# Kernel tuning notes

Hardware: AMD Instinct MI355X
Metric: run time of the kernel (lower is better)

## Reference

```python
import jax, jax.numpy as jnp
import numpy as np

N_NODES = 100000
N_EDGES = 1600000
IN_DIM, HID, OUT_DIM = 512, 32, 40


def setup_inputs() -> dict:
    key = jax.random.key(0)
    ks = jax.random.split(key, 6)
    x = jax.random.normal(ks[0], (N_NODES, IN_DIM), dtype=jnp.float32)
    edge_index = jax.random.randint(ks[1], (2, N_EDGES), 0, N_NODES, dtype=jnp.int64)
    # Glorot-ish init for the linear weights
    W1 = jax.random.normal(ks[2], (IN_DIM, HID), dtype=jnp.float32) / np.sqrt(IN_DIM)
    b1 = jnp.zeros((HID,), dtype=jnp.float32)
    W2 = jax.random.normal(ks[3], (HID, OUT_DIM), dtype=jnp.float32) / np.sqrt(HID)
    b2 = jnp.zeros((OUT_DIM,), dtype=jnp.float32)
    return {"x": x, "edge_index": edge_index, "W1": W1, "b1": b1, "W2": W2, "b2": b2}


def gcn_conv(x, W, b, src, dst, n_nodes):
    """PyG GCNConv: h = D^{-1/2} (A + I) D^{-1/2} (x W) + b."""
    h = x @ W  # linear transform first (reduces edge-level traffic)
    # add self-loops
    loop = jnp.arange(n_nodes, dtype=src.dtype)
    s = jnp.concatenate([src, loop])
    d = jnp.concatenate([dst, loop])
    # symmetric normalization from in-degree (including self-loops)
    deg = jax.ops.segment_sum(jnp.ones_like(d, dtype=h.dtype), d, num_segments=n_nodes)
    dinv = jnp.where(deg > 0, jax.lax.rsqrt(deg), 0.0)
    norm = dinv[s] * dinv[d]  # [E+N]
    msg = h[s] * norm[:, None]  # gather + scale
    out = jax.ops.segment_sum(msg, d, num_segments=n_nodes)  # scatter-add
    return out + b


def reference(x, edge_index, W1, b1, W2, b2):
    src, dst = edge_index[0], edge_index[1]
    n = x.shape[0]
    h = jax.nn.relu(gcn_conv(x, W1, b1, src, dst, n))
    # dropout is identity in eval mode (reference runs in eval)
    out = gcn_conv(h, W2, b2, src, dst, n)
    return out
```

## Files before the change

### kernel.cpp

```cpp
#include <hip/hip_runtime.h>
#include <hip/hip_bf16.h>

#define N_IN 512
#define HID 32
#define OUTD 40

typedef __attribute__((ext_vector_type(8))) short bf16x8;
typedef __attribute__((ext_vector_type(4))) float f32x4;


__global__ void k_init(int* __restrict__ csr, int tot4, int n4, int n,
                       float* __restrict__ g1, float* __restrict__ p,
                       int* __restrict__ cnt)
{
    int i = blockIdx.x * blockDim.x + threadIdx.x;
    if (i < tot4) {
        int4 v = make_int4(n, n, n, n);
        *(int4*)&csr[(size_t)i * 4] = v;
    }
    if (i < n4) {
        int4 z4 = make_int4(0, 0, 0, 0);
        *(int4*)&cnt[(size_t)i * 4] = z4;
    }
    if (blockIdx.x == 0) {
        float4 z = make_float4(0.f, 0.f, 0.f, 0.f);
        if (threadIdx.x < 8)
            *(float4*)&g1[(size_t)n * HID + threadIdx.x * 4] = z;
        else if (threadIdx.x < 16)
            *(float4*)&p[(size_t)n * HID + (threadIdx.x - 8) * 4] = z;
    }
}

__global__ void k_count(const int* __restrict__ dst, int* cnt, int e) {
    int i = (blockIdx.x * blockDim.x + threadIdx.x) * 4;
    if (i + 3 < e) {
        int4 d4 = *(const int4*)&dst[i];
        atomicAdd(&cnt[d4.x], 1);
        atomicAdd(&cnt[d4.y], 1);
        atomicAdd(&cnt[d4.z], 1);
        atomicAdd(&cnt[d4.w], 1);
    } else {
        for (int k = i; k < e; k++) atomicAdd(&cnt[dst[k]], 1);
    }
}

__global__ __launch_bounds__(256) void k_scan1(const int* __restrict__ cnt,
                                               int* __restrict__ offs,
                                               int* __restrict__ bsums, int n)
{
    __shared__ int sm[256];
    int t = threadIdx.x;
    int base = blockIdx.x * 1024 + t * 4;
    int a0 = (base + 0 < n) ? cnt[base + 0] : 0;
    int a1 = (base + 1 < n) ? cnt[base + 1] : 0;
    int a2 = (base + 2 < n) ? cnt[base + 2] : 0;
    int a3 = (base + 3 < n) ? cnt[base + 3] : 0;
    int d0 = (a0 + 15) & ~15;
    int d1 = (a1 + 15) & ~15;
    int d2 = (a2 + 15) & ~15;
    int d3 = (a3 + 15) & ~15;
    int s = d0 + d1 + d2 + d3;
    sm[t] = s;
    __syncthreads();
#pragma unroll
    for (int off = 1; off < 256; off <<= 1) {
        int v = (t >= off) ? sm[t - off] : 0;
        __syncthreads();
        sm[t] += v;
        __syncthreads();
    }
    int excl = sm[t] - s;
    if (base + 0 < n) offs[base + 0] = excl;
    if (base + 1 < n) offs[base + 1] = excl + d0;
    if (base + 2 < n) offs[base + 2] = excl + d0 + d1;
    if (base + 3 < n) offs[base + 3] = excl + d0 + d1 + d2;
    if (t == 255) bsums[blockIdx.x] = sm[255];
}

__global__ __launch_bounds__(256) void k_scan2(int* bsums, int nb)
{
    __shared__ int sm[256];
    int t = threadIdx.x;
    int s = (t < nb) ? bsums[t] : 0;
    sm[t] = s;
    __syncthreads();
#pragma unroll
    for (int off = 1; off < 256; off <<= 1) {
        int v = (t >= off) ? sm[t - off] : 0;
        __syncthreads();
        sm[t] += v;
        __syncthreads();
    }
    if (t < nb) bsums[t] = sm[t] - s;
}

__global__ void k_scan3(int* __restrict__ offs, int* __restrict__ cursor,
                        const int* __restrict__ bsums, const int* __restrict__ cnt,
                        float* __restrict__ dinv, int n)
{
    int i = blockIdx.x * blockDim.x + threadIdx.x;
    if (i >= n) return;
    int o = offs[i] + bsums[i >> 10];
    offs[i] = o;
    cursor[i] = o;
    dinv[i] = rsqrtf((float)(cnt[i] + 1));
}

__global__ void k_fill(const int* __restrict__ src, const int* __restrict__ dst,
                       int* cursor, int* __restrict__ csr, int e)
{
    int i = (blockIdx.x * blockDim.x + threadIdx.x) * 4;
    if (i >= e) return;
    if (i + 3 < e) {
        int4 d4 = *(const int4*)&dst[i];
        int4 s4 = *(const int4*)&src[i];
        int dd[4] = {d4.x, d4.y, d4.z, d4.w};
        int ss[4] = {s4.x, s4.y, s4.z, s4.w};
#pragma unroll
        for (int k = 0; k < 4; k++) {
            int p = atomicAdd(&cursor[dd[k]], 1);
            csr[p] = ss[k];
        }
    } else {
        for (int k = i; k < e; k++) {
            int p = atomicAdd(&cursor[dst[k]], 1);
            csr[p] = src[k];
        }
    }
}

__global__ void k_convw(const float* __restrict__ W, unsigned short* __restrict__ wfh,
                        unsigned short* __restrict__ wfl)
{
    int idx = blockIdx.x * blockDim.x + threadIdx.x;
    int j     = idx & 7;
    int lane  = (idx >> 3) & 63;
    int ntile = (idx >> 9) & 1;
    int kstep = idx >> 10;
    int k    = kstep * 32 + (lane >> 4) * 8 + j;
    int ncol = ntile * 16 + (lane & 15);
    float v = W[k * HID + ncol];
    unsigned u = __builtin_bit_cast(unsigned, v);
    unsigned short h = (unsigned short)(u >> 16);
    float hv = __builtin_bit_cast(float, u & 0xFFFF0000u);
    float rem = v - hv;
    unsigned ur = __builtin_bit_cast(unsigned, rem);
    ur += 0x7FFF + ((ur >> 16) & 1);
    wfh[idx] = h;
    wfl[idx] = (unsigned short)(ur >> 16);
}

__global__ __launch_bounds__(256) void k_gemm1(
    const float* __restrict__ x,
    const unsigned short* __restrict__ wfh, const unsigned short* __restrict__ wfl,
    const float* __restrict__ dinv, float* __restrict__ g1, int n)
{
    const int t    = threadIdx.x;
    const int lane = t & 63;
    const int wave = t >> 6;
    const int m    = lane & 15;
    const int quad = lane >> 4;
    const int row0 = blockIdx.x * 64 + wave * 16;

    int arow = row0 + m;
    if (arow >= n) arow = n - 1;
    const float* xp = x + (size_t)arow * N_IN + quad * 8;

    f32x4 acc0 = {0.f, 0.f, 0.f, 0.f};
    f32x4 acc1 = {0.f, 0.f, 0.f, 0.f};

    for (int ks = 0; ks < 16; ks++) {
        float4 xa = *(const float4*)(xp + ks * 32);
        float4 xb = *(const float4*)(xp + ks * 32 + 4);
        float xe[8] = {xa.x, xa.y, xa.z, xa.w, xb.x, xb.y, xb.z, xb.w};
        bf16x8 ah, al;
#pragma unroll
        for (int j = 0; j < 8; j++) {
            unsigned u = __builtin_bit_cast(unsigned, xe[j]);
            ah[j] = (short)(u >> 16);
            float hv = __builtin_bit_cast(float, u & 0xFFFF0000u);
            float rem = xe[j] - hv;
            unsigned ur = __builtin_bit_cast(unsigned, rem);
            ur += 0x7FFF + ((ur >> 16) & 1);
            al[j] = (short)(ur >> 16);
        }
        bf16x8 bh0 = *(const bf16x8*)(wfh + ((size_t)(ks * 2 + 0) * 64 + lane) * 8);
        bf16x8 bh1 = *(const bf16x8*)(wfh + ((size_t)(ks * 2 + 1) * 64 + lane) * 8);
        bf16x8 bl0 = *(const bf16x8*)(wfl + ((size_t)(ks * 2 + 0) * 64 + lane) * 8);
        bf16x8 bl1 = *(const bf16x8*)(wfl + ((size_t)(ks * 2 + 1) * 64 + lane) * 8);

        acc0 = __builtin_amdgcn_mfma_f32_16x16x32_bf16(ah, bh0, acc0, 0, 0, 0);
        acc0 = __builtin_amdgcn_mfma_f32_16x16x32_bf16(al, bh0, acc0, 0, 0, 0);
        acc0 = __builtin_amdgcn_mfma_f32_16x16x32_bf16(ah, bl0, acc0, 0, 0, 0);
        acc1 = __builtin_amdgcn_mfma_f32_16x16x32_bf16(ah, bh1, acc1, 0, 0, 0);
        acc1 = __builtin_amdgcn_mfma_f32_16x16x32_bf16(al, bh1, acc1, 0, 0, 0);
        acc1 = __builtin_amdgcn_mfma_f32_16x16x32_bf16(ah, bl1, acc1, 0, 0, 0);
    }

#pragma unroll
    for (int r = 0; r < 4; r++) {
        int row = row0 + quad * 4 + r;
        if (row < n) {
            float dv = dinv[row];
            g1[(size_t)row * HID + m]      = acc0[r] * dv;
            g1[(size_t)row * HID + 16 + m] = acc1[r] * dv;
        }
    }
}


__global__ void k_agg1(const int* __restrict__ csr, const int* __restrict__ offs,
                       const int* __restrict__ cnt, const float* __restrict__ g,
                       const float* __restrict__ dinv, const float* __restrict__ b1,
                       float* __restrict__ p, int n)
{
    int gid = blockIdx.x * blockDim.x + threadIdx.x;
    int r  = gid >> 4;
    int sl = gid & 15;
    if (r >= n) return;
    int s0 = offs[r];
    int dp = (cnt[r] + 15) & ~15;
    int half = sl >> 3;
    int c = sl & 7;
    const float* gc = g + c * 4;
    float4 acc = make_float4(0.f, 0.f, 0.f, 0.f);
    if (half == 0) acc = *(const float4*)&gc[(size_t)r * HID];
    for (int b = 0; b < dp; b += 16) {
        int s = csr[s0 + b + sl];
#pragma unroll
        for (int jj = 0; jj < 8; jj++) {
            int sj = __shfl(s, jj + (half << 3), 16);
            float4 v = *(const float4*)&gc[(size_t)sj * HID];
            acc.x += v.x; acc.y += v.y; acc.z += v.z; acc.w += v.w;
        }
    }
    float4 o;
    o.x = __shfl(acc.x, sl ^ 8, 16);
    o.y = __shfl(acc.y, sl ^ 8, 16);
    o.z = __shfl(acc.z, sl ^ 8, 16);
    o.w = __shfl(acc.w, sl ^ 8, 16);
    if (half == 0) {
        float dv = dinv[r];
        float4 bv = *(const float4*)&b1[c * 4];
        float4 hp;
        hp.x = dv * fmaxf((acc.x + o.x) * dv + bv.x, 0.f);
        hp.y = dv * fmaxf((acc.y + o.y) * dv + bv.y, 0.f);
        hp.z = dv * fmaxf((acc.z + o.z) * dv + bv.z, 0.f);
        hp.w = dv * fmaxf((acc.w + o.w) * dv + bv.w, 0.f);
        *(float4*)&p[(size_t)r * HID + c * 4] = hp;
    }
}

__global__ void k_agg2_out(const int* __restrict__ csr, const int* __restrict__ offs,
                           const int* __restrict__ cnt, const float* __restrict__ g,
                           const float* __restrict__ dinv, const float* __restrict__ W2,
                           const float* __restrict__ b2, float* __restrict__ out, int n)
{
    int gid = blockIdx.x * blockDim.x + threadIdx.x;
    int r  = gid >> 4;
    int sl = gid & 15;
    if (r >= n) return;
    int s0 = offs[r];
    int dp = (cnt[r] + 15) & ~15;
    int half = sl >> 3;
    int c = sl & 7;
    const float* gc = g + c * 4;
    float4 acc = make_float4(0.f, 0.f, 0.f, 0.f);
    if (half == 0) acc = *(const float4*)&gc[(size_t)r * HID];
    for (int b = 0; b < dp; b += 16) {
        int s = csr[s0 + b + sl];
#pragma unroll
        for (int jj = 0; jj < 8; jj++) {
            int sj = __shfl(s, jj + (half << 3), 16);
            float4 v = *(const float4*)&gc[(size_t)sj * HID];
            acc.x += v.x; acc.y += v.y; acc.z += v.z; acc.w += v.w;
        }
    }
    float4 o;
    o.x = __shfl(acc.x, sl ^ 8, 16);
    o.y = __shfl(acc.y, sl ^ 8, 16);
    o.z = __shfl(acc.z, sl ^ 8, 16);
    o.w = __shfl(acc.w, sl ^ 8, 16);
    float dv = dinv[r];
    float h0 = (acc.x + o.x) * dv;
    float h1 = (acc.y + o.y) * dv;
    float h2 = (acc.z + o.z) * dv;
    float h3 = (acc.w + o.w) * dv;

    int oc = (sl < 10) ? sl * 4 : 0;
    float4 ov = *(const float4*)&b2[oc];
#pragma unroll
    for (int k4 = 0; k4 < 8; k4++) {
        float a0 = __shfl(h0, k4, 16);
        float a1 = __shfl(h1, k4, 16);
        float a2 = __shfl(h2, k4, 16);
        float a3 = __shfl(h3, k4, 16);
        float4 w0 = *(const float4*)&W2[(4 * k4 + 0) * OUTD + oc];
        float4 w1 = *(const float4*)&W2[(4 * k4 + 1) * OUTD + oc];
        float4 w2 = *(const float4*)&W2[(4 * k4 + 2) * OUTD + oc];
        float4 w3 = *(const float4*)&W2[(4 * k4 + 3) * OUTD + oc];
        ov.x += a0 * w0.x + a1 * w1.x + a2 * w2.x + a3 * w3.x;
        ov.y += a0 * w0.y + a1 * w1.y + a2 * w2.y + a3 * w3.y;
        ov.z += a0 * w0.z + a1 * w1.z + a2 * w2.z + a3 * w3.z;
        ov.w += a0 * w0.w + a1 * w1.w + a2 * w2.w + a3 * w3.w;
    }
    if (sl < 10) *(float4*)&out[(size_t)r * OUTD + sl * 4] = ov;
}

extern "C" void kernel_launch(void* const* d_in, const int* in_sizes, int n_in,
                              void* d_out, int out_size, void* d_ws, size_t ws_size,
                              hipStream_t stream)
{
    const float* x  = (const float*)d_in[0];
    const int*   ei = (const int*)d_in[1];
    const float* W1 = (const float*)d_in[2];
    const float* b1 = (const float*)d_in[3];
    const float* W2 = (const float*)d_in[4];
    const float* b2 = (const float*)d_in[5];
    float* out = (float*)d_out;

    const int n = in_sizes[0] / N_IN;
    const int e = in_sizes[1] / 2;
    const int* src = ei;
    const int* dst = ei + e;

    const int csr_cap = e + 16 * n;

    char* w = (char*)d_ws;
    float* dinv   = (float*)w;            w += sizeof(float) * (size_t)((n + 3) & ~3);
    float* g1     = (float*)w;            w += sizeof(float) * (size_t)(n + 1) * HID;
    float* p      = (float*)w;            w += sizeof(float) * (size_t)(n + 1) * HID;
    int*   cnt    = (int*)w;              w += sizeof(int) * (size_t)((n + 3) & ~3);
    int*   offs   = (int*)w;              w += sizeof(int) * (size_t)((n + 3) & ~3);
    int*   cursor = (int*)w;              w += sizeof(int) * (size_t)((n + 3) & ~3);
    int*   bsums  = (int*)w;              w += sizeof(int) * 1024;
    unsigned short* wfh = (unsigned short*)w;  w += sizeof(unsigned short) * 16384;
    unsigned short* wfl = (unsigned short*)w;  w += sizeof(unsigned short) * 16384;
    int*   csr    = (int*)w;              w += sizeof(int) * (size_t)((csr_cap + 3) & ~3);

    const int nb = (n + 1023) / 1024;
    const int ec = (e + 3) / 4;
    const int n4 = (n + 3) / 4;
    const int tot4 = (csr_cap + 3) / 4;
    const int initN = (tot4 > n4) ? tot4 : n4;

    k_init<<<(initN + 255) / 256, 256, 0, stream>>>(csr, tot4, n4, n, g1, p, cnt);
    k_count<<<(ec + 255) / 256, 256, 0, stream>>>(dst, cnt, e);
    k_scan1<<<nb, 256, 0, stream>>>(cnt, offs, bsums, n);
    k_scan2<<<1, 256, 0, stream>>>(bsums, nb);
    k_scan3<<<(n + 255) / 256, 256, 0, stream>>>(offs, cursor, bsums, cnt, dinv, n);
    k_fill<<<(ec + 255) / 256, 256, 0, stream>>>(src, dst, cursor, csr, e);

    k_convw<<<64, 256, 0, stream>>>(W1, wfh, wfl);

    k_gemm1<<<(n + 63) / 64, 256, 0, stream>>>(x, wfh, wfl, dinv, g1, n);

    int t16 = n * 16;
    k_agg1<<<(t16 + 255) / 256, 256, 0, stream>>>(csr, offs, cnt, g1, dinv, b1, p, n);
    k_agg2_out<<<(t16 + 255) / 256, 256, 0, stream>>>(csr, offs, cnt, p, dinv, W2, b2, out, n);
}
```

Measured before the change: 596.1 us.

## Privatize degree counters and record atomic ranks to remove fill-phase atomics

Degree counting now uses eight privatized counter copies selected by block index, and each edge records its copy id and returned atomic rank. A per-node pass turns the copies into per-copy bases, and a new position kernel computes each edge's CSR slot from offset, base and rank. The fill then scatters without atomics. This aims to cut atomic contention and drop the second atomic pass over a cursor array, at the cost of extra kernels, an E-sized rank buffer and more memory traffic.

```diff
diff --git a/kernel.cpp b/kernel.cpp
--- a/kernel.cpp
+++ b/kernel.cpp
@@ -4,23 +4,23 @@
 #define N_IN 512
 #define HID 32
 #define OUTD 40
+#define NCOPY 8
 
 typedef __attribute__((ext_vector_type(8))) short bf16x8;
 typedef __attribute__((ext_vector_type(4))) float f32x4;
 
 
-__global__ void k_init(int* __restrict__ csr, int tot4, int n4, int n,
-                       float* __restrict__ g1, float* __restrict__ p,
-                       int* __restrict__ cnt)
+__global__ void k_init(int* __restrict__ csr, int tot4, int* __restrict__ cnt8,
+                       int n8_4, int n, float* __restrict__ g1, float* __restrict__ p)
 {
     int i = blockIdx.x * blockDim.x + threadIdx.x;
     if (i < tot4) {
         int4 v = make_int4(n, n, n, n);
         *(int4*)&csr[(size_t)i * 4] = v;
     }
-    if (i < n4) {
+    if (i < n8_4) {
         int4 z4 = make_int4(0, 0, 0, 0);
-        *(int4*)&cnt[(size_t)i * 4] = z4;
+        *(int4*)&cnt8[(size_t)i * 4] = z4;
     }
     if (blockIdx.x == 0) {
         float4 z = make_float4(0.f, 0.f, 0.f, 0.f);
@@ -31,17 +31,40 @@
     }
 }
 
-__global__ void k_count(const int* __restrict__ dst, int* cnt, int e) {
+__global__ void k_count(const int* __restrict__ dst, int* __restrict__ cnt8,
+                        int* __restrict__ rankp, int n, int e)
+{
+    int c = blockIdx.x & (NCOPY - 1);
+    int* mycnt = cnt8 + (size_t)c * n;
     int i = (blockIdx.x * blockDim.x + threadIdx.x) * 4;
     if (i + 3 < e) {
         int4 d4 = *(const int4*)&dst[i];
-        atomicAdd(&cnt[d4.x], 1);
-        atomicAdd(&cnt[d4.y], 1);
-        atomicAdd(&cnt[d4.z], 1);
-        atomicAdd(&cnt[d4.w], 1);
-    } else {
-        for (int k = i; k < e; k++) atomicAdd(&cnt[dst[k]], 1);
-    }
+        int r0 = atomicAdd(&mycnt[d4.x], 1);
+        int r1 = atomicAdd(&mycnt[d4.y], 1);
+        int r2 = atomicAdd(&mycnt[d4.z], 1);
+        int r3 = atomicAdd(&mycnt[d4.w], 1);
+        int hc = c << 24;
+        *(int4*)&rankp[i] = make_int4(hc | r0, hc | r1, hc | r2, hc | r3);
+    } else if (i < e) {
+        for (int k = i; k < e; k++) {
+            int r = atomicAdd(&mycnt[dst[k]], 1);
+            rankp[k] = (c << 24) | r;
+        }
+    }
+}
+
+__global__ void k_bases(int* __restrict__ cnt8, int* __restrict__ cnt, int n)
+{
+    int d = blockIdx.x * blockDim.x + threadIdx.x;
+    if (d >= n) return;
+    int s = 0;
+#pragma unroll
+    for (int c = 0; c < NCOPY; c++) {
+        int v = cnt8[(size_t)c * n + d];
+        cnt8[(size_t)c * n + d] = s;
+        s += v;
+    }
+    cnt[d] = s;
 }
 
 __global__ __launch_bounds__(256) void k_scan1(const int* __restrict__ cnt,
@@ -94,38 +117,60 @@
     if (t < nb) bsums[t] = sm[t] - s;
 }
 
-__global__ void k_scan3(int* __restrict__ offs, int* __restrict__ cursor,
-                        const int* __restrict__ bsums, const int* __restrict__ cnt,
-                        float* __restrict__ dinv, int n)
+__global__ void k_scan3(int* __restrict__ offs, const int* __restrict__ bsums,
+                        const int* __restrict__ cnt, float* __restrict__ dinv, int n)
 {
     int i = blockIdx.x * blockDim.x + threadIdx.x;
     if (i >= n) return;
-    int o = offs[i] + bsums[i >> 10];
-    offs[i] = o;
-    cursor[i] = o;
+    offs[i] = offs[i] + bsums[i >> 10];
     dinv[i] = rsqrtf((float)(cnt[i] + 1));
 }
 
-__global__ void k_fill(const int* __restrict__ src, const int* __restrict__ dst,
-                       int* cursor, int* __restrict__ csr, int e)
+__global__ void k_pos(const int* __restrict__ dst, const int* __restrict__ offs,
+                      const int* __restrict__ cnt8, int* __restrict__ rankp,
+                      int n, int e)
 {
     int i = (blockIdx.x * blockDim.x + threadIdx.x) * 4;
     if (i >= e) return;
     if (i + 3 < e) {
         int4 d4 = *(const int4*)&dst[i];
-        int4 s4 = *(const int4*)&src[i];
+        int4 rp = *(const int4*)&rankp[i];
         int dd[4] = {d4.x, d4.y, d4.z, d4.w};
-        int ss[4] = {s4.x, s4.y, s4.z, s4.w};
+        int rr[4] = {rp.x, rp.y, rp.z, rp.w};
+        int pp[4];
 #pragma unroll
         for (int k = 0; k < 4; k++) {
-            int p = atomicAdd(&cursor[dd[k]], 1);
-            csr[p] = ss[k];
-        }
+            int d = dd[k];
+            int c = ((unsigned)rr[k]) >> 24;
+            int r = rr[k] & 0xFFFFFF;
+            pp[k] = offs[d] + cnt8[(size_t)c * n + d] + r;
+        }
+        *(int4*)&rankp[i] = make_int4(pp[0], pp[1], pp[2], pp[3]);
     } else {
         for (int k = i; k < e; k++) {
-            int p = atomicAdd(&cursor[dst[k]], 1);
-            csr[p] = src[k];
-        }
+            int d = dst[k];
+            int r = rankp[k];
+            int c = ((unsigned)r) >> 24;
+            r &= 0xFFFFFF;
+            rankp[k] = offs[d] + cnt8[(size_t)c * n + d] + r;
+        }
+    }
+}
+
+__global__ void k_fill(const int* __restrict__ src, const int* __restrict__ pos,
+                       int* __restrict__ csr, int e)
+{
+    int i = (blockIdx.x * blockDim.x + threadIdx.x) * 4;
+    if (i >= e) return;
+    if (i + 3 < e) {
+        int4 p4 = *(const int4*)&pos[i];
+        int4 s4 = *(const int4*)&src[i];
+        csr[p4.x] = s4.x;
+        csr[p4.y] = s4.y;
+        csr[p4.z] = s4.z;
+        csr[p4.w] = s4.w;
+    } else {
+        for (int k = i; k < e; k++) csr[pos[k]] = src[k];
     }
 }
 
@@ -332,7 +377,8 @@
     float* p      = (float*)w;            w += sizeof(float) * (size_t)(n + 1) * HID;
     int*   cnt    = (int*)w;              w += sizeof(int) * (size_t)((n + 3) & ~3);
     int*   offs   = (int*)w;              w += sizeof(int) * (size_t)((n + 3) & ~3);
-    int*   cursor = (int*)w;              w += sizeof(int) * (size_t)((n + 3) & ~3);
+    int*   cnt8   = (int*)w;              w += sizeof(int) * (size_t)NCOPY * ((n + 3) & ~3);
+    int*   rankp  = (int*)w;              w += sizeof(int) * (size_t)((e + 3) & ~3);
     int*   bsums  = (int*)w;              w += sizeof(int) * 1024;
     unsigned short* wfh = (unsigned short*)w;  w += sizeof(unsigned short) * 16384;
     unsigned short* wfl = (unsigned short*)w;  w += sizeof(unsigned short) * 16384;
@@ -340,16 +386,18 @@
 
     const int nb = (n + 1023) / 1024;
     const int ec = (e + 3) / 4;
-    const int n4 = (n + 3) / 4;
+    const int n8_4 = (NCOPY * n + 3) / 4;
     const int tot4 = (csr_cap + 3) / 4;
-    const int initN = (tot4 > n4) ? tot4 : n4;
-
-    k_init<<<(initN + 255) / 256, 256, 0, stream>>>(csr, tot4, n4, n, g1, p, cnt);
-    k_count<<<(ec + 255) / 256, 256, 0, stream>>>(dst, cnt, e);
+    const int initN = (tot4 > n8_4) ? tot4 : n8_4;
+
+    k_init<<<(initN + 255) / 256, 256, 0, stream>>>(csr, tot4, cnt8, n8_4, n, g1, p);
+    k_count<<<(ec + 255) / 256, 256, 0, stream>>>(dst, cnt8, rankp, n, e);
+    k_bases<<<(n + 255) / 256, 256, 0, stream>>>(cnt8, cnt, n);
     k_scan1<<<nb, 256, 0, stream>>>(cnt, offs, bsums, n);
     k_scan2<<<1, 256, 0, stream>>>(bsums, nb);
-    k_scan3<<<(n + 255) / 256, 256, 0, stream>>>(offs, cursor, bsums, cnt, dinv, n);
-    k_fill<<<(ec + 255) / 256, 256, 0, stream>>>(src, dst, cursor, csr, e);
+    k_scan3<<<(n + 255) / 256, 256, 0, stream>>>(offs, bsums, cnt, dinv, n);
+    k_pos<<<(ec + 255) / 256, 256, 0, stream>>>(dst, offs, cnt8, rankp, n, e);
+    k_fill<<<(ec + 255) / 256, 256, 0, stream>>>(src, rankp, csr, e);
 
     k_convw<<<64, 256, 0, stream>>>(W1, wfh, wfl);
 
```

Measured after the change: 510.1 us. 14.4% less time.
